# Kernel optimization log

Measured on AMD Instinct MI355X. Metric: run time of the kernel, lower is better.

Reference implementation:

```python
import jax, jax.numpy as jnp
import numpy as np

A0 = 0.529177249
SIGMA = jnp.array([0.5515909, 1.8886297, 1.3225029, 1.2316629, 2.1884933, 1.7750372, 1.3677907, 1.3820058], dtype=jnp.float32)

N_MOL, N_ATOM, AEV_LEN = 256, 384, 384
DIMS = [160, 128, 96]


def _mlp(x, W1, b1, W2, b2, W3, b3, W4, b4):
    celu = lambda v: jax.nn.celu(v, alpha=0.1)
    h = celu(x @ W1.T + b1)
    h = celu(h @ W2.T + b2)
    h = celu(h @ W3.T + b3)
    return jax.nn.softplus(h @ W4.T + b4)  # (Nn, 1)


def setup_inputs() -> dict:
    key = jax.random.key(0)
    ks = jax.random.split(key, 12)
    species = jax.random.randint(ks[0], (N_MOL, N_ATOM), 0, 8)
    # pad the tail of each molecule (species == -1)
    species = species.at[:, N_ATOM - 64:].set(-1)
    coordinates = jax.random.normal(ks[1], (N_MOL, N_ATOM, 3), dtype=jnp.float32) * 3.0
    net_charge = jax.random.normal(ks[2], (N_MOL,), dtype=jnp.float32)
    aev = jax.random.normal(ks[3], (N_MOL, N_ATOM, AEV_LEN), dtype=jnp.float32)
    in_dim = AEV_LEN + 2
    d1, d2, d3 = DIMS
    s = 0.05
    W1 = jax.random.normal(ks[4], (d1, in_dim), dtype=jnp.float32) * s
    b1 = jnp.zeros((d1,), dtype=jnp.float32)
    W2 = jax.random.normal(ks[5], (d2, d1), dtype=jnp.float32) * s
    b2 = jnp.zeros((d2,), dtype=jnp.float32)
    W3 = jax.random.normal(ks[6], (d3, d2), dtype=jnp.float32) * s
    b3 = jnp.zeros((d3,), dtype=jnp.float32)
    W4 = jax.random.normal(ks[7], (1, d3), dtype=jnp.float32) * s
    b4 = jnp.zeros((1,), dtype=jnp.float32)
    return {"species": species, "coordinates": coordinates, "net_charge": net_charge,
            "aev": aev, "W1": W1, "b1": b1, "W2": W2, "b2": b2,
            "W3": W3, "b3": b3, "W4": W4, "b4": b4}


def reference(species, coordinates, net_charge, aev, W1, b1, W2, b2, W3, b3, W4, b4):
    N, n = species.shape
    # pairwise distances in atomic units (eps avoids div-by-zero on diagonal)
    diff = coordinates[:, None, :, :] - coordinates[:, :, None, :]  # (N,n,n,3)
    distances = jnp.sqrt(jnp.sum(diff * diff, axis=-1) + 1e-16) / A0  # (N,n,n)

    padding_mask = (species != -1).astype(coordinates.dtype)  # (N,n)
    pair_mask = padding_mask[:, :, None] * padding_mask[:, None, :]  # (N,n,n)
    num_atoms = padding_mask.sum(axis=1)  # (N,)

    # ESP kernel j_ij (constant across iterations)
    sig = SIGMA[species]  # negative padding index wraps to last sigma, as in torch
    sig_sqsum = jnp.maximum(sig[:, None, :] ** 2 + sig[:, :, None] ** 2, 1e-8)
    j_ij = jax.lax.erf(distances / jnp.sqrt(2.0 * sig_sqsum)) / distances  # (N,n,n)
    diag_mask = 1.0 - jnp.eye(n, dtype=coordinates.dtype)
    j_masked = j_ij * pair_mask * diag_mask[None]  # fuse masks once

    mask_flat = species.reshape(-1) != -1  # (N*n,)
    aev_flat = aev.reshape(N * n, -1)
    pred_charges = jnp.zeros((N * n,), dtype=coordinates.dtype)
    esp = jnp.zeros((N * n,), dtype=coordinates.dtype)

    for _ in range(4):
        feats = jnp.concatenate(
            [aev_flat, pred_charges[:, None], esp[:, None]], axis=1)  # (Nn, aev+2)
        chi_all = _mlp(feats, W1, b1, W2, b2, W3, b3, W4, b4)[:, 0]
        chi = jnp.where(mask_flat, chi_all, 0.0)  # padded atoms keep 0 (masked_scatter)
        chi_copy = chi.reshape(N, n)
        chi_sum = chi_copy.sum(axis=-1)  # (N,)
        k_net = 1.0 + jnp.abs(net_charge) / chi_sum
        chi_mean = chi_sum / num_atoms
        k_p = jnp.where(net_charge > 0, k_net, 1.0)
        k_n = jnp.where(net_charge < 0, k_net, 1.0)
        iter_charges = (-k_n[:, None] * chi_copy + (k_p * chi_mean)[:, None]) * padding_mask
        # esp_j = sum_i q_i * j_ij[i, j] (masked)
        esp2d = jnp.sum(iter_charges[:, :, None] * j_masked, axis=1)  # (N,n)
        pred_charges = iter_charges.reshape(-1)
        esp = esp2d.reshape(-1)

    return species, pred_charges.reshape(N, n)
```

## Files before the change

kernel.cpp:

```cpp
#include <hip/hip_runtime.h>
#include <math.h>

#define NMOL 256
#define NATOM 384
#define NN (NMOL*NATOM)
#define A0C  0.529177249f
#define A0_INV (1.0f/0.529177249f)

typedef short bf16x8 __attribute__((ext_vector_type(8)));
typedef float f32x4  __attribute__((ext_vector_type(4)));
typedef _Float16 h16x8 __attribute__((ext_vector_type(8)));

__constant__ float c_sigma[8] = {0.5515909f, 1.8886297f, 1.3225029f, 1.2316629f,
                                 2.1884933f, 1.7750372f, 1.3677907f, 1.3820058f};

__device__ __forceinline__ short f2b(float f) {
    unsigned u = __float_as_uint(f);
    u = (u + 0x7fffu + ((u >> 16) & 1u)) >> 16;
    return (short)u;
}
__device__ __forceinline__ float b2f(short s) {
    return __uint_as_float(((unsigned)(unsigned short)s) << 16);
}
__device__ __forceinline__ float celu01(float v) {
    float e = __builtin_amdgcn_exp2f(v * 14.426950408889634f);
    return v > 0.f ? v : fmaf(0.1f, e, -0.1f);
}
__device__ __forceinline__ bf16x8 cvt8(f32x4 a, f32x4 b) {
    bf16x8 r;
    r[0] = f2b(a.x); r[1] = f2b(a.y); r[2] = f2b(a.z); r[3] = f2b(a.w);
    r[4] = f2b(b.x); r[5] = f2b(b.y); r[6] = f2b(b.z); r[7] = f2b(b.w);
    return r;
}

__device__ __forceinline__ float erf_fast(float x) {
    float t = __builtin_amdgcn_rcpf(fmaf(0.3275911f, x, 1.0f));
    float p = fmaf(t, 1.061405429f, -1.453152027f);
    p = fmaf(t, p, 1.421413741f);
    p = fmaf(t, p, -0.284496736f);
    p = fmaf(t, p, 0.254829592f);
    p = p * t;
    float e = __builtin_amdgcn_exp2f(-x * x * 1.4426950408889634f);
    return fmaf(-p, e, 1.0f);
}

template<int N, int K>
__global__ __launch_bounds__(256, 4)
void gemm0_k(const float* __restrict__ A, const short* __restrict__ Bw,
             const float* __restrict__ bias, short* __restrict__ Cout)
{
    constexpr int NK = K / 32;
    constexpr int NF = N / 32;
    constexpr int N2 = N / 2;
    constexpr int AROW = 40, BROW = 40;
    constexpr int ASZ = 64 * AROW;
    constexpr int BSZ = N * BROW;
    constexpr int AB  = 2 * ASZ + 2 * BSZ;
    constexpr int CSZ = 64 * N;
    constexpr int SM  = AB > CSZ ? AB : CSZ;
    constexpr int NB  = (N * 4 + 255) / 256;

    __shared__ short smem[SM];
    short* As0 = smem;
    short* As1 = smem + ASZ;
    short* Bs0 = smem + 2 * ASZ;
    short* Bs1 = smem + 2 * ASZ + BSZ;
    short* Cs  = smem;

    const int t    = threadIdx.x;
    const int lane = t & 63;
    const int wave = t >> 6;
    const int wm   = wave >> 1, wn = wave & 1;
    const int l15  = lane & 15, l4 = lane >> 4;
    const int m0   = blockIdx.x * 64;
    const int arow = t >> 2, aseg = t & 3;
    const float* a_f32 = A + ((size_t)m0 + arow) * K + aseg * 8;

    f32x4 af0, af1;
    bf16x8 br[NB];

    auto loadA = [&](int k0) {
        af0 = *(const f32x4*)(a_f32 + k0);
        af1 = *(const f32x4*)(a_f32 + k0 + 4);
    };
    auto loadB = [&](int k0) {
        #pragma unroll
        for (int ci = 0; ci < NB; ++ci) {
            int c = ci * 256 + t;
            if ((N * 4) % 256 == 0 || c < N * 4) {
                int row = c >> 2, half = c & 3;
                br[ci] = *(const bf16x8*)(Bw + (size_t)row * K + k0 + half * 8);
            }
        }
    };
    auto writeA = [&](short* dst) {
        *(bf16x8*)&dst[arow * AROW + aseg * 8] = cvt8(af0, af1);
    };
    auto writeB = [&](short* dst) {
        #pragma unroll
        for (int ci = 0; ci < NB; ++ci) {
            int c = ci * 256 + t;
            if ((N * 4) % 256 == 0 || c < N * 4) {
                int row = c >> 2, half = c & 3;
                *(bf16x8*)&dst[row * BROW + half * 8] = br[ci];
            }
        }
    };

    f32x4 acc[2][NF] = {};

    loadA(0); loadB(0);
    writeA(As0); writeB(Bs0);
    __syncthreads();

    int cur = 0;
    for (int ks = 0; ks < NK; ++ks) {
        if (ks + 1 < NK) { loadA((ks + 1) * 32); loadB((ks + 1) * 32); }
        short* Ac = cur ? As1 : As0;
        short* Bc = cur ? Bs1 : Bs0;
        bf16x8 a[2];
        #pragma unroll
        for (int mf = 0; mf < 2; ++mf)
            a[mf] = *(const bf16x8*)&Ac[(wm * 32 + mf * 16 + l15) * AROW + l4 * 8];
        #pragma unroll
        for (int nf = 0; nf < NF; ++nf) {
            bf16x8 b = *(const bf16x8*)&Bc[(wn * N2 + nf * 16 + l15) * BROW + l4 * 8];
            #pragma unroll
            for (int mf = 0; mf < 2; ++mf)
                acc[mf][nf] = __builtin_amdgcn_mfma_f32_16x16x32_bf16(a[mf], b, acc[mf][nf], 0, 0, 0);
        }
        if (ks + 1 < NK) {
            writeA(cur ? As0 : As1);
            writeB(cur ? Bs0 : Bs1);
            __syncthreads();
            cur ^= 1;
        }
    }
    __syncthreads();

    #pragma unroll
    for (int nf = 0; nf < NF; ++nf) {
        int col = wn * N2 + nf * 16 + l15;
        float bc = bias[col];
        #pragma unroll
        for (int mf = 0; mf < 2; ++mf)
            #pragma unroll
            for (int r = 0; r < 4; ++r)
                Cs[(wm * 32 + mf * 16 + l4 * 4 + r) * N + col] = f2b(acc[mf][nf][r] + bc);
    }
    __syncthreads();
    #pragma unroll
    for (int i = 0; i < NF; ++i) {
        int c = i * 256 + t;
        *(bf16x8*)(Cout + (size_t)m0 * N + c * 8) = *(const bf16x8*)&Cs[c * 8];
    }
}

__global__ __launch_bounds__(256, 4)
void mlp23_kernel(const short* __restrict__ h1p, const short* __restrict__ W2b,
                  const float* __restrict__ b2, const short* __restrict__ W3b,
                  const float* __restrict__ b3, const float* __restrict__ W4,
                  const float* __restrict__ b4,
                  const float* __restrict__ qv, const float* __restrict__ espv,
                  const float* __restrict__ w1qp, const float* __restrict__ w1ep,
                  const int* __restrict__ species, float* __restrict__ chi)
{
    constexpr int K1 = 160, K2 = 128, N3 = 96;
    constexpr int H2ROW = 140;

    __shared__ short H2[64 * H2ROW];
    __shared__ float wq_s[K1], we_s[K1], w4_s[N3], b3_s[N3];
    __shared__ float chp[2][64];

    const int t    = threadIdx.x;
    const int lane = t & 63;
    const int wave = t >> 6;
    const int wm   = wave >> 1, wn = wave & 1;
    const int l15  = lane & 15, l4 = lane >> 4;
    const int m0   = blockIdx.x * 64;

    if (t < K1) { wq_s[t] = w1qp[t]; we_s[t] = w1ep[t]; }
    if (t < N3) { w4_s[t] = W4[t]; b3_s[t] = b3[t]; }

    int rowg[2];
    float qrow[2], erow[2];
    #pragma unroll
    for (int mf = 0; mf < 2; ++mf) {
        rowg[mf] = m0 + wm * 32 + mf * 16 + l15;
        qrow[mf] = qv[rowg[mf]];
        erow[mf] = espv[rowg[mf]] + espv[NN + rowg[mf]]
                 + espv[2 * (size_t)NN + rowg[mf]] + espv[3 * (size_t)NN + rowg[mf]];
    }
    __syncthreads();

    f32x4 acc[2][4] = {};
    #pragma unroll
    for (int ks = 0; ks < 5; ++ks) {
        const int k0 = ks * 32 + l4 * 8;
        f32x4 wq0 = *(const f32x4*)&wq_s[k0];
        f32x4 wq1 = *(const f32x4*)&wq_s[k0 + 4];
        f32x4 we0 = *(const f32x4*)&we_s[k0];
        f32x4 we1 = *(const f32x4*)&we_s[k0 + 4];
        bf16x8 a[2];
        #pragma unroll
        for (int mf = 0; mf < 2; ++mf) {
            bf16x8 h = *(const bf16x8*)(h1p + (size_t)rowg[mf] * K1 + k0);
            #pragma unroll
            for (int j = 0; j < 4; ++j) {
                float v = b2f(h[j]) + qrow[mf] * wq0[j] + erow[mf] * we0[j];
                a[mf][j] = f2b(celu01(v));
                float v2 = b2f(h[j + 4]) + qrow[mf] * wq1[j] + erow[mf] * we1[j];
                a[mf][j + 4] = f2b(celu01(v2));
            }
        }
        #pragma unroll
        for (int nf = 0; nf < 4; ++nf) {
            bf16x8 b = *(const bf16x8*)(W2b + (size_t)(wn * 64 + nf * 16 + l15) * K1 + k0);
            #pragma unroll
            for (int mf = 0; mf < 2; ++mf)
                acc[mf][nf] = __builtin_amdgcn_mfma_f32_16x16x32_bf16(a[mf], b, acc[mf][nf], 0, 0, 0);
        }
    }

    #pragma unroll
    for (int nf = 0; nf < 4; ++nf) {
        int col = wn * 64 + nf * 16 + l15;
        float bc = b2[col];
        #pragma unroll
        for (int mf = 0; mf < 2; ++mf)
            #pragma unroll
            for (int r = 0; r < 4; ++r)
                H2[(wm * 32 + mf * 16 + l4 * 4 + r) * H2ROW + col] =
                    f2b(celu01(acc[mf][nf][r] + bc));
    }
    __syncthreads();

    f32x4 acc2[2][3] = {};
    #pragma unroll
    for (int ks = 0; ks < 4; ++ks) {
        bf16x8 a[2];
        #pragma unroll
        for (int mf = 0; mf < 2; ++mf)
            a[mf] = *(const bf16x8*)&H2[(wm * 32 + mf * 16 + l15) * H2ROW + ks * 32 + l4 * 8];
        #pragma unroll
        for (int nf = 0; nf < 3; ++nf) {
            bf16x8 b = *(const bf16x8*)(W3b + (size_t)(wn * 48 + nf * 16 + l15) * K2 + ks * 32 + l4 * 8);
            #pragma unroll
            for (int mf = 0; mf < 2; ++mf)
                acc2[mf][nf] = __builtin_amdgcn_mfma_f32_16x16x32_bf16(a[mf], b, acc2[mf][nf], 0, 0, 0);
        }
    }

    float val[2][4];
    #pragma unroll
    for (int mf = 0; mf < 2; ++mf)
        #pragma unroll
        for (int r = 0; r < 4; ++r) val[mf][r] = 0.f;
    #pragma unroll
    for (int nf = 0; nf < 3; ++nf) {
        int col = wn * 48 + nf * 16 + l15;
        float bc = b3_s[col];
        float wc = w4_s[col];
        #pragma unroll
        for (int mf = 0; mf < 2; ++mf)
            #pragma unroll
            for (int r = 0; r < 4; ++r)
                val[mf][r] += celu01(acc2[mf][nf][r] + bc) * wc;
    }
    #pragma unroll
    for (int off = 1; off < 16; off <<= 1)
        #pragma unroll
        for (int mf = 0; mf < 2; ++mf)
            #pragma unroll
            for (int r = 0; r < 4; ++r)
                val[mf][r] += __shfl_xor(val[mf][r], off, 64);
    if (l15 == 0) {
        #pragma unroll
        for (int mf = 0; mf < 2; ++mf)
            #pragma unroll
            for (int r = 0; r < 4; ++r)
                chp[wn][wm * 32 + mf * 16 + l4 * 4 + r] = val[mf][r];
    }
    __syncthreads();
    if (t < 64) {
        float s = chp[0][t] + chp[1][t] + b4[0];
        s = fmaxf(s, 0.f) + log1pf(expf(-fabsf(s)));
        chi[m0 + t] = (species[m0 + t] != -1) ? s : 0.f;
    }
}

__global__ __launch_bounds__(384)
void jbuild_kernel(const float* __restrict__ coords, const int* __restrict__ species,
                   _Float16* __restrict__ J)
{
    __shared__ float cx[NATOM], cy[NATOM], cz[NATOM], s2[NATOM], mk[NATOM];
    int m = blockIdx.x, it0 = blockIdx.y * 48;
    int j = threadIdx.x;
    int idx = m * NATOM + j;
    float rx = coords[(size_t)idx * 3 + 0];
    float ry = coords[(size_t)idx * 3 + 1];
    float rz = coords[(size_t)idx * 3 + 2];
    int sp = species[idx];
    float sig = c_sigma[sp < 0 ? 7 : sp];
    cx[j] = rx; cy[j] = ry; cz[j] = rz;
    s2[j] = sig * sig;
    float maskj = (sp != -1) ? 1.f : 0.f;
    mk[j] = maskj;
    __syncthreads();
    float s2j = s2[j];
    #pragma unroll 4
    for (int ii = 0; ii < 48; ++ii) {
        int i = it0 + ii;
        float dx = cx[i] - rx, dy = cy[i] - ry, dz = cz[i] - rz;
        float d2 = fmaf(dx, dx, fmaf(dy, dy, dz * dz)) + 1e-16f;
        float rs = __builtin_amdgcn_rsqf(d2);
        float d  = d2 * rs * A0_INV;
        float ss = fmaxf(s2[i] + s2j, 1e-8f);
        float x  = d * __builtin_amdgcn_rsqf(2.f * ss);
        float val = erf_fast(x) * rs * A0C;
        val *= maskj * mk[i];
        val = (i == j) ? 0.f : val;
        J[((size_t)m * NATOM + i) * NATOM + j] = (_Float16)val;
    }
}

template<bool DO_MV>
__global__ __launch_bounds__(384)
void espmv_kernel(const float* __restrict__ chi, const int* __restrict__ species,
                  const float* __restrict__ netq, const _Float16* __restrict__ J,
                  float* __restrict__ q, float* __restrict__ esp_part)
{
    __shared__ float pw[6], pwc[6];
    __shared__ float qs[DO_MV ? 96 : 1];
    __shared__ float part[DO_MV ? 8 : 1][DO_MV ? 384 : 1];
    int m = blockIdx.x, ic = blockIdx.y;
    int t = threadIdx.x;
    int lane = t & 63, wv = t >> 6;
    int idx = m * NATOM + t;
    float c = chi[idx];
    int sp = species[idx];
    float mask = (sp != -1) ? 1.f : 0.f;
    float sc = c, sm = mask;
    #pragma unroll
    for (int off = 1; off < 64; off <<= 1) {
        sc += __shfl_xor(sc, off, 64);
        sm += __shfl_xor(sm, off, 64);
    }
    if (lane == 0) { pw[wv] = sc; pwc[wv] = sm; }
    __syncthreads();
    float chi_sum = pw[0] + pw[1] + pw[2] + pw[3] + pw[4] + pw[5];
    float na      = pwc[0] + pwc[1] + pwc[2] + pwc[3] + pwc[4] + pwc[5];
    float Q = netq[m];
    float k_net = 1.f + fabsf(Q) / chi_sum;
    float chi_mean = chi_sum / na;
    float k_p = (Q > 0.f) ? k_net : 1.f;
    float k_n = (Q < 0.f) ? k_net : 1.f;
    float qj = (-k_n * c + k_p * chi_mean) * mask;
    if (ic == 0) q[idx] = qj;

    if (DO_MV) {
        if (t >= ic * 96 && t < ic * 96 + 96) qs[t - ic * 96] = qj;
        __syncthreads();
        int jv = t % 48, isub = t / 48;
        int j0 = jv * 8;
        float acc[8] = {};
        #pragma unroll 4
        for (int k = 0; k < 12; ++k) {
            int il = isub * 12 + k;
            int i = ic * 96 + il;
            h16x8 h = *(const h16x8*)&J[((size_t)m * NATOM + i) * NATOM + j0];
            float qi = qs[il];
            #pragma unroll
            for (int r = 0; r < 8; ++r) acc[r] = fmaf(qi, (float)h[r], acc[r]);
        }
        #pragma unroll
        for (int r = 0; r < 8; ++r) part[isub][j0 + r] = acc[r];
        __syncthreads();
        float s = 0.f;
        #pragma unroll
        for (int g = 0; g < 8; ++g) s += part[g][t];
        esp_part[(size_t)ic * NN + idx] = s;
    }
}

template<bool DO_ESP>
__global__ __launch_bounds__(384)
void espq_kernel(const float* __restrict__ chi, const int* __restrict__ species,
                 const float* __restrict__ netq, const float* __restrict__ coords,
                 float* __restrict__ q, float* __restrict__ esp)
{
    __shared__ float red[512], redc[512];
    __shared__ float cx[NATOM], cy[NATOM], cz[NATOM], s2[NATOM], qs[NATOM];
    int m = blockIdx.x, j = threadIdx.x;
    int idx = m * NATOM + j;
    float c = chi[idx];
    int sp = species[idx];
    float mask = (sp != -1) ? 1.f : 0.f;
    red[j] = c; redc[j] = mask;
    if (j < 128) { red[NATOM + j] = 0.f; redc[NATOM + j] = 0.f; }
    __syncthreads();
    for (int s = 256; s > 0; s >>= 1) {
        if (j < s) { red[j] += red[j + s]; redc[j] += redc[j + s]; }
        __syncthreads();
    }
    float chi_sum = red[0], na = redc[0];
    float Q = netq[m];
    float k_net = 1.f + fabsf(Q) / chi_sum;
    float chi_mean = chi_sum / na;
    float k_p = (Q > 0.f) ? k_net : 1.f;
    float k_n = (Q < 0.f) ? k_net : 1.f;
    float qj = (-k_n * c + k_p * chi_mean) * mask;
    q[idx] = qj;

    if (DO_ESP) {
        float rx = coords[(size_t)idx * 3 + 0];
        float ry = coords[(size_t)idx * 3 + 1];
        float rz = coords[(size_t)idx * 3 + 2];
        cx[j] = rx; cy[j] = ry; cz[j] = rz;
        float sig = c_sigma[sp < 0 ? 7 : sp];
        s2[j] = sig * sig;
        qs[j] = qj;
        __syncthreads();
        float s2j = s2[j];
        float acc = 0.f;
        for (int i = 0; i < NATOM; ++i) {
            float dx = cx[i] - rx, dy = cy[i] - ry, dz = cz[i] - rz;
            float d2 = fmaf(dx, dx, fmaf(dy, dy, dz * dz)) + 1e-16f;
            float rs = __builtin_amdgcn_rsqf(d2);
            float d  = d2 * rs * A0_INV;
            float ss = fmaxf(s2[i] + s2j, 1e-8f);
            float x  = d * __builtin_amdgcn_rsqf(2.f * ss);
            float val = erf_fast(x) * rs * A0C;
            acc += (i == j) ? 0.f : qs[i] * val;
        }
        esp[idx] = (mask != 0.f) ? acc : 0.f;
    }
}

__global__ __launch_bounds__(256)
void wcvt_kernel(const float* __restrict__ W1, const float* __restrict__ W2,
                 const float* __restrict__ W3,
                 short* __restrict__ W1b, short* __restrict__ W2b,
                 short* __restrict__ W3b, float* __restrict__ w1q,
                 float* __restrict__ w1e)
{
    int i = blockIdx.x * 256 + threadIdx.x;
    if (i < 160 * 384) {
        int r = i / 384, cc = i % 384;
        W1b[i] = f2b(W1[(size_t)r * 386 + cc]);
    }
    int j = i - 160 * 384;
    if (j >= 0 && j < 128 * 160) W2b[j] = f2b(W2[j]);
    int k2 = j - 128 * 160;
    if (k2 >= 0 && k2 < 96 * 128) W3b[k2] = f2b(W3[k2]);
    if (i < 160) {
        w1q[i] = W1[(size_t)i * 386 + 384];
        w1e[i] = W1[(size_t)i * 386 + 385];
    }
}

__global__ __launch_bounds__(256)
void out_kernel(const int* __restrict__ species, const float* __restrict__ q,
                float* __restrict__ out)
{
    int i = blockIdx.x * 256 + threadIdx.x;
    out[i] = (float)species[i];
    out[NN + i] = q[i];
}

extern "C" void kernel_launch(void* const* d_in, const int* in_sizes, int n_in,
                              void* d_out, int out_size, void* d_ws, size_t ws_size,
                              hipStream_t stream)
{
    const int*   species = (const int*)  d_in[0];
    const float* coords  = (const float*)d_in[1];
    const float* netq    = (const float*)d_in[2];
    const float* aev     = (const float*)d_in[3];
    const float* W1 = (const float*)d_in[4];
    const float* b1 = (const float*)d_in[5];
    const float* W2 = (const float*)d_in[6];
    const float* b2 = (const float*)d_in[7];
    const float* W3 = (const float*)d_in[8];
    const float* b3 = (const float*)d_in[9];
    const float* W4 = (const float*)d_in[10];
    const float* b4 = (const float*)d_in[11];

    float* q    = (float*)d_ws;
    float* chi  = q + NN;
    float* espp = chi + NN;
    float* w1q  = espp + 4 * (size_t)NN;
    float* w1e  = w1q + 160;
    short* W1b  = (short*)(w1e + 160);
    short* W2b  = W1b + 160 * 384;
    short* W3b  = W2b + 128 * 160;
    short* h1p  = W3b + 96 * 128;
    _Float16* J = (_Float16*)(h1p + (size_t)NN * 160);

    const size_t NEED = (size_t)((char*)(J + (size_t)NN * 384) - (char*)d_ws);
    const bool use_J = (ws_size >= NEED);

    hipMemsetAsync(d_ws, 0, 6 * (size_t)NN * sizeof(float), stream);
    wcvt_kernel<<<(160 * 384 + 128 * 160 + 96 * 128 + 255) / 256, 256, 0, stream>>>(
        W1, W2, W3, W1b, W2b, W3b, w1q, w1e);

    if (use_J)
        jbuild_kernel<<<dim3(NMOL, 8), 384, 0, stream>>>(coords, species, J);

    gemm0_k<160, 384><<<NN / 64, 256, 0, stream>>>(aev, W1b, b1, h1p);

    for (int it = 0; it < 4; ++it) {
        mlp23_kernel<<<NN / 64, 256, 0, stream>>>(
            h1p, W2b, b2, W3b, b3, W4, b4, q, espp, w1q, w1e, species, chi);
        if (use_J) {
            if (it < 3)
                espmv_kernel<true><<<dim3(NMOL, 4), 384, 0, stream>>>(
                    chi, species, netq, J, q, espp);
            else
                espmv_kernel<false><<<dim3(NMOL, 1), 384, 0, stream>>>(
                    chi, species, netq, J, q, espp);
        } else {
            if (it < 3)
                espq_kernel<true><<<NMOL, 384, 0, stream>>>(
                    chi, species, netq, coords, q, espp);
            else
                espq_kernel<false><<<NMOL, 384, 0, stream>>>(
                    chi, species, netq, coords, q, espp);
        }
    }

    out_kernel<<<NN / 256, 256, 0, stream>>>(species, q, (float*)d_out);
}
```

Before: 257.4 us.

## Fuse all charge-equilibration iterations into one persistent per-molecule kernel

Replaces the per-iteration launches (MLP layers 2-4, the J-matrix build, the ESP matvec, the charge update and the output write) with a single kernel that runs one block per molecule. The block keeps h1 in registers and W2/W3 in LDS, and recomputes the ESP pair kernel on the fly each iteration instead of storing a precomputed fp16 J matrix. This removes the J build, its global read traffic, the intermediate q/chi/esp global buffers and the memset, plus about a dozen launches. In exchange, only 256 blocks of 512 threads run, which may underfill the GPU, and the erf-based pair kernel is recomputed three times per molecule.

```diff
diff --git a/kernel.cpp b/kernel.cpp
--- a/kernel.cpp
+++ b/kernel.cpp
@@ -9,7 +9,6 @@
 
 typedef short bf16x8 __attribute__((ext_vector_type(8)));
 typedef float f32x4  __attribute__((ext_vector_type(4)));
-typedef _Float16 h16x8 __attribute__((ext_vector_type(8)));
 
 __constant__ float c_sigma[8] = {0.5515909f, 1.8886297f, 1.3225029f, 1.2316629f,
                                  2.1884933f, 1.7750372f, 1.3677907f, 1.3820058f};
@@ -156,284 +155,231 @@
     }
 }
 
-__global__ __launch_bounds__(256, 4)
-void mlp23_kernel(const short* __restrict__ h1p, const short* __restrict__ W2b,
-                  const float* __restrict__ b2, const short* __restrict__ W3b,
-                  const float* __restrict__ b3, const float* __restrict__ W4,
-                  const float* __restrict__ b4,
-                  const float* __restrict__ qv, const float* __restrict__ espv,
-                  const float* __restrict__ w1qp, const float* __restrict__ w1ep,
-                  const int* __restrict__ species, float* __restrict__ chi)
+#define MROW  164
+#define W3ROW 132
+
+__global__ __launch_bounds__(512, 2)
+void mega_kernel(const short* __restrict__ h1p, const short* __restrict__ W2b,
+                 const float* __restrict__ b2v, const short* __restrict__ W3b,
+                 const float* __restrict__ b3v, const float* __restrict__ W4,
+                 const float* __restrict__ b4, const float* __restrict__ w1qp,
+                 const float* __restrict__ w1ep, const int* __restrict__ species,
+                 const float* __restrict__ netq, const float* __restrict__ coords,
+                 float* __restrict__ out)
 {
-    constexpr int K1 = 160, K2 = 128, N3 = 96;
-    constexpr int H2ROW = 140;
-
-    __shared__ short H2[64 * H2ROW];
-    __shared__ float wq_s[K1], we_s[K1], w4_s[N3], b3_s[N3];
-    __shared__ float chp[2][64];
+    __shared__ short BUF[128 * MROW];
+    __shared__ short W2s[128 * MROW];
+    __shared__ short W3s[96 * W3ROW];
+    __shared__ float wq_s[160], we_s[160], b2_s[128], b3_s[96], w4_s[96];
+    __shared__ float cxs[NATOM], cys[NATOM], czs[NATOM], s2s[NATOM], msk_s[NATOM];
+    __shared__ float chi_s[NATOM], q_s[NATOM], esp_s[NATOM];
+    __shared__ float chp[2][128];
+    __shared__ float red_s[8], redc_s[8];
 
     const int t    = threadIdx.x;
     const int lane = t & 63;
-    const int wave = t >> 6;
-    const int wm   = wave >> 1, wn = wave & 1;
+    const int wv   = t >> 6;
+    const int rg   = wv >> 1;
+    const int ch   = wv & 1;
     const int l15  = lane & 15, l4 = lane >> 4;
-    const int m0   = blockIdx.x * 64;
-
-    if (t < K1) { wq_s[t] = w1qp[t]; we_s[t] = w1ep[t]; }
-    if (t < N3) { w4_s[t] = W4[t]; b3_s[t] = b3[t]; }
-
-    int rowg[2];
-    float qrow[2], erow[2];
+    const int m    = blockIdx.x;
+
+    if (t < 160)                { wq_s[t] = w1qp[t]; we_s[t] = w1ep[t]; }
+    else if (t < 288)           b2_s[t - 160] = b2v[t - 160];
+    else if (t < 384)           { b3_s[t - 288] = b3v[t - 288]; w4_s[t - 288] = W4[t - 288]; }
+    if (t < NATOM) {
+        int idx = m * NATOM + t;
+        cxs[t] = coords[(size_t)idx * 3 + 0];
+        cys[t] = coords[(size_t)idx * 3 + 1];
+        czs[t] = coords[(size_t)idx * 3 + 2];
+        int sp = species[idx];
+        float sig = c_sigma[sp < 0 ? 7 : sp];
+        s2s[t] = sig * sig;
+        msk_s[t] = (sp != -1) ? 1.f : 0.f;
+        q_s[t] = 0.f; esp_s[t] = 0.f;
+    }
     #pragma unroll
-    for (int mf = 0; mf < 2; ++mf) {
-        rowg[mf] = m0 + wm * 32 + mf * 16 + l15;
-        qrow[mf] = qv[rowg[mf]];
-        erow[mf] = espv[rowg[mf]] + espv[NN + rowg[mf]]
-                 + espv[2 * (size_t)NN + rowg[mf]] + espv[3 * (size_t)NN + rowg[mf]];
+    for (int i = 0; i < 5; ++i) {
+        int id = t + i * 512;
+        int row = id / 20, seg = id % 20;
+        *(bf16x8*)&W2s[row * MROW + seg * 8] = *(const bf16x8*)(W2b + (size_t)row * 160 + seg * 8);
+    }
+    #pragma unroll
+    for (int i = 0; i < 3; ++i) {
+        int id = t + i * 512;
+        int row = id / 16, seg = id % 16;
+        *(bf16x8*)&W3s[row * W3ROW + seg * 8] = *(const bf16x8*)(W3b + (size_t)row * 128 + seg * 8);
+    }
+
+    bf16x8 hraw[3][2][5];
+    #pragma unroll
+    for (int c = 0; c < 3; ++c) {
+        __syncthreads();
+        #pragma unroll
+        for (int i = 0; i < 5; ++i) {
+            int id = t + i * 512;
+            int row = id / 20, seg = id % 20;
+            *(bf16x8*)&BUF[row * MROW + seg * 8] =
+                *(const bf16x8*)(h1p + ((size_t)m * NATOM + c * 128 + row) * 160 + seg * 8);
+        }
+        __syncthreads();
+        #pragma unroll
+        for (int mf = 0; mf < 2; ++mf)
+            #pragma unroll
+            for (int ks = 0; ks < 5; ++ks)
+                hraw[c][mf][ks] = *(const bf16x8*)&BUF[(rg * 32 + mf * 16 + l15) * MROW + ks * 32 + l4 * 8];
     }
     __syncthreads();
 
-    f32x4 acc[2][4] = {};
-    #pragma unroll
-    for (int ks = 0; ks < 5; ++ks) {
-        const int k0 = ks * 32 + l4 * 8;
-        f32x4 wq0 = *(const f32x4*)&wq_s[k0];
-        f32x4 wq1 = *(const f32x4*)&wq_s[k0 + 4];
-        f32x4 we0 = *(const f32x4*)&we_s[k0];
-        f32x4 we1 = *(const f32x4*)&we_s[k0 + 4];
-        bf16x8 a[2];
-        #pragma unroll
-        for (int mf = 0; mf < 2; ++mf) {
-            bf16x8 h = *(const bf16x8*)(h1p + (size_t)rowg[mf] * K1 + k0);
-            #pragma unroll
-            for (int j = 0; j < 4; ++j) {
-                float v = b2f(h[j]) + qrow[mf] * wq0[j] + erow[mf] * we0[j];
-                a[mf][j] = f2b(celu01(v));
-                float v2 = b2f(h[j + 4]) + qrow[mf] * wq1[j] + erow[mf] * we1[j];
-                a[mf][j + 4] = f2b(celu01(v2));
-            }
-        }
-        #pragma unroll
-        for (int nf = 0; nf < 4; ++nf) {
-            bf16x8 b = *(const bf16x8*)(W2b + (size_t)(wn * 64 + nf * 16 + l15) * K1 + k0);
-            #pragma unroll
-            for (int mf = 0; mf < 2; ++mf)
-                acc[mf][nf] = __builtin_amdgcn_mfma_f32_16x16x32_bf16(a[mf], b, acc[mf][nf], 0, 0, 0);
-        }
-    }
-
-    #pragma unroll
-    for (int nf = 0; nf < 4; ++nf) {
-        int col = wn * 64 + nf * 16 + l15;
-        float bc = b2[col];
-        #pragma unroll
-        for (int mf = 0; mf < 2; ++mf)
-            #pragma unroll
-            for (int r = 0; r < 4; ++r)
-                H2[(wm * 32 + mf * 16 + l4 * 4 + r) * H2ROW + col] =
-                    f2b(celu01(acc[mf][nf][r] + bc));
-    }
-    __syncthreads();
-
-    f32x4 acc2[2][3] = {};
-    #pragma unroll
-    for (int ks = 0; ks < 4; ++ks) {
-        bf16x8 a[2];
-        #pragma unroll
-        for (int mf = 0; mf < 2; ++mf)
-            a[mf] = *(const bf16x8*)&H2[(wm * 32 + mf * 16 + l15) * H2ROW + ks * 32 + l4 * 8];
-        #pragma unroll
-        for (int nf = 0; nf < 3; ++nf) {
-            bf16x8 b = *(const bf16x8*)(W3b + (size_t)(wn * 48 + nf * 16 + l15) * K2 + ks * 32 + l4 * 8);
-            #pragma unroll
-            for (int mf = 0; mf < 2; ++mf)
-                acc2[mf][nf] = __builtin_amdgcn_mfma_f32_16x16x32_bf16(a[mf], b, acc2[mf][nf], 0, 0, 0);
-        }
-    }
-
-    float val[2][4];
-    #pragma unroll
-    for (int mf = 0; mf < 2; ++mf)
-        #pragma unroll
-        for (int r = 0; r < 4; ++r) val[mf][r] = 0.f;
-    #pragma unroll
-    for (int nf = 0; nf < 3; ++nf) {
-        int col = wn * 48 + nf * 16 + l15;
-        float bc = b3_s[col];
-        float wc = w4_s[col];
-        #pragma unroll
-        for (int mf = 0; mf < 2; ++mf)
-            #pragma unroll
-            for (int r = 0; r < 4; ++r)
-                val[mf][r] += celu01(acc2[mf][nf][r] + bc) * wc;
-    }
-    #pragma unroll
-    for (int off = 1; off < 16; off <<= 1)
-        #pragma unroll
-        for (int mf = 0; mf < 2; ++mf)
-            #pragma unroll
-            for (int r = 0; r < 4; ++r)
-                val[mf][r] += __shfl_xor(val[mf][r], off, 64);
-    if (l15 == 0) {
-        #pragma unroll
-        for (int mf = 0; mf < 2; ++mf)
-            #pragma unroll
-            for (int r = 0; r < 4; ++r)
-                chp[wn][wm * 32 + mf * 16 + l4 * 4 + r] = val[mf][r];
-    }
-    __syncthreads();
-    if (t < 64) {
-        float s = chp[0][t] + chp[1][t] + b4[0];
-        s = fmaxf(s, 0.f) + log1pf(expf(-fabsf(s)));
-        chi[m0 + t] = (species[m0 + t] != -1) ? s : 0.f;
-    }
-}
-
-__global__ __launch_bounds__(384)
-void jbuild_kernel(const float* __restrict__ coords, const int* __restrict__ species,
-                   _Float16* __restrict__ J)
-{
-    __shared__ float cx[NATOM], cy[NATOM], cz[NATOM], s2[NATOM], mk[NATOM];
-    int m = blockIdx.x, it0 = blockIdx.y * 48;
-    int j = threadIdx.x;
-    int idx = m * NATOM + j;
-    float rx = coords[(size_t)idx * 3 + 0];
-    float ry = coords[(size_t)idx * 3 + 1];
-    float rz = coords[(size_t)idx * 3 + 2];
-    int sp = species[idx];
-    float sig = c_sigma[sp < 0 ? 7 : sp];
-    cx[j] = rx; cy[j] = ry; cz[j] = rz;
-    s2[j] = sig * sig;
-    float maskj = (sp != -1) ? 1.f : 0.f;
-    mk[j] = maskj;
-    __syncthreads();
-    float s2j = s2[j];
-    #pragma unroll 4
-    for (int ii = 0; ii < 48; ++ii) {
-        int i = it0 + ii;
-        float dx = cx[i] - rx, dy = cy[i] - ry, dz = cz[i] - rz;
-        float d2 = fmaf(dx, dx, fmaf(dy, dy, dz * dz)) + 1e-16f;
-        float rs = __builtin_amdgcn_rsqf(d2);
-        float d  = d2 * rs * A0_INV;
-        float ss = fmaxf(s2[i] + s2j, 1e-8f);
-        float x  = d * __builtin_amdgcn_rsqf(2.f * ss);
-        float val = erf_fast(x) * rs * A0C;
-        val *= maskj * mk[i];
-        val = (i == j) ? 0.f : val;
-        J[((size_t)m * NATOM + i) * NATOM + j] = (_Float16)val;
-    }
-}
-
-template<bool DO_MV>
-__global__ __launch_bounds__(384)
-void espmv_kernel(const float* __restrict__ chi, const int* __restrict__ species,
-                  const float* __restrict__ netq, const _Float16* __restrict__ J,
-                  float* __restrict__ q, float* __restrict__ esp_part)
-{
-    __shared__ float pw[6], pwc[6];
-    __shared__ float qs[DO_MV ? 96 : 1];
-    __shared__ float part[DO_MV ? 8 : 1][DO_MV ? 384 : 1];
-    int m = blockIdx.x, ic = blockIdx.y;
-    int t = threadIdx.x;
-    int lane = t & 63, wv = t >> 6;
-    int idx = m * NATOM + t;
-    float c = chi[idx];
-    int sp = species[idx];
-    float mask = (sp != -1) ? 1.f : 0.f;
-    float sc = c, sm = mask;
-    #pragma unroll
-    for (int off = 1; off < 64; off <<= 1) {
-        sc += __shfl_xor(sc, off, 64);
-        sm += __shfl_xor(sm, off, 64);
-    }
-    if (lane == 0) { pw[wv] = sc; pwc[wv] = sm; }
-    __syncthreads();
-    float chi_sum = pw[0] + pw[1] + pw[2] + pw[3] + pw[4] + pw[5];
-    float na      = pwc[0] + pwc[1] + pwc[2] + pwc[3] + pwc[4] + pwc[5];
-    float Q = netq[m];
-    float k_net = 1.f + fabsf(Q) / chi_sum;
-    float chi_mean = chi_sum / na;
-    float k_p = (Q > 0.f) ? k_net : 1.f;
-    float k_n = (Q < 0.f) ? k_net : 1.f;
-    float qj = (-k_n * c + k_p * chi_mean) * mask;
-    if (ic == 0) q[idx] = qj;
-
-    if (DO_MV) {
-        if (t >= ic * 96 && t < ic * 96 + 96) qs[t - ic * 96] = qj;
+    const float b4v = b4[0];
+    const float Q   = netq[m];
+
+    for (int it = 0; it < 4; ++it) {
+        #pragma unroll
+        for (int c = 0; c < 3; ++c) {
+            float qrow[2], erow[2];
+            #pragma unroll
+            for (int mf = 0; mf < 2; ++mf) {
+                int rl = c * 128 + rg * 32 + mf * 16 + l15;
+                qrow[mf] = q_s[rl];
+                erow[mf] = esp_s[rl];
+            }
+            f32x4 acc[2][4] = {};
+            #pragma unroll
+            for (int ks = 0; ks < 5; ++ks) {
+                const int k0 = ks * 32 + l4 * 8;
+                f32x4 wq0 = *(const f32x4*)&wq_s[k0];
+                f32x4 wq1 = *(const f32x4*)&wq_s[k0 + 4];
+                f32x4 we0 = *(const f32x4*)&we_s[k0];
+                f32x4 we1 = *(const f32x4*)&we_s[k0 + 4];
+                bf16x8 a[2];
+                #pragma unroll
+                for (int mf = 0; mf < 2; ++mf) {
+                    bf16x8 h = hraw[c][mf][ks];
+                    #pragma unroll
+                    for (int j = 0; j < 4; ++j) {
+                        float v  = b2f(h[j])     + qrow[mf] * wq0[j] + erow[mf] * we0[j];
+                        float v2 = b2f(h[j + 4]) + qrow[mf] * wq1[j] + erow[mf] * we1[j];
+                        a[mf][j]     = f2b(celu01(v));
+                        a[mf][j + 4] = f2b(celu01(v2));
+                    }
+                }
+                #pragma unroll
+                for (int nf = 0; nf < 4; ++nf) {
+                    bf16x8 b = *(const bf16x8*)&W2s[(ch * 64 + nf * 16 + l15) * MROW + k0];
+                    #pragma unroll
+                    for (int mf = 0; mf < 2; ++mf)
+                        acc[mf][nf] = __builtin_amdgcn_mfma_f32_16x16x32_bf16(a[mf], b, acc[mf][nf], 0, 0, 0);
+                }
+            }
+            #pragma unroll
+            for (int nf = 0; nf < 4; ++nf) {
+                int col = ch * 64 + nf * 16 + l15;
+                float bc = b2_s[col];
+                #pragma unroll
+                for (int mf = 0; mf < 2; ++mf)
+                    #pragma unroll
+                    for (int r = 0; r < 4; ++r)
+                        BUF[(rg * 32 + mf * 16 + l4 * 4 + r) * MROW + col] =
+                            f2b(celu01(acc[mf][nf][r] + bc));
+            }
+            __syncthreads();
+            f32x4 acc2[2][3] = {};
+            #pragma unroll
+            for (int ks = 0; ks < 4; ++ks) {
+                bf16x8 a2[2];
+                #pragma unroll
+                for (int mf = 0; mf < 2; ++mf)
+                    a2[mf] = *(const bf16x8*)&BUF[(rg * 32 + mf * 16 + l15) * MROW + ks * 32 + l4 * 8];
+                #pragma unroll
+                for (int nf = 0; nf < 3; ++nf) {
+                    bf16x8 b = *(const bf16x8*)&W3s[(ch * 48 + nf * 16 + l15) * W3ROW + ks * 32 + l4 * 8];
+                    #pragma unroll
+                    for (int mf = 0; mf < 2; ++mf)
+                        acc2[mf][nf] = __builtin_amdgcn_mfma_f32_16x16x32_bf16(a2[mf], b, acc2[mf][nf], 0, 0, 0);
+                }
+            }
+            float val[2][4] = {};
+            #pragma unroll
+            for (int nf = 0; nf < 3; ++nf) {
+                int col = ch * 48 + nf * 16 + l15;
+                float bc = b3_s[col], wc = w4_s[col];
+                #pragma unroll
+                for (int mf = 0; mf < 2; ++mf)
+                    #pragma unroll
+                    for (int r = 0; r < 4; ++r)
+                        val[mf][r] += celu01(acc2[mf][nf][r] + bc) * wc;
+            }
+            #pragma unroll
+            for (int off = 1; off < 16; off <<= 1)
+                #pragma unroll
+                for (int mf = 0; mf < 2; ++mf)
+                    #pragma unroll
+                    for (int r = 0; r < 4; ++r)
+                        val[mf][r] += __shfl_xor(val[mf][r], off, 64);
+            if (l15 == 0) {
+                #pragma unroll
+                for (int mf = 0; mf < 2; ++mf)
+                    #pragma unroll
+                    for (int r = 0; r < 4; ++r)
+                        chp[ch][rg * 32 + mf * 16 + l4 * 4 + r] = val[mf][r];
+            }
+            __syncthreads();
+            if (t < 128) {
+                float s = chp[0][t] + chp[1][t] + b4v;
+                s = fmaxf(s, 0.f) + log1pf(expf(-fabsf(s)));
+                chi_s[c * 128 + t] = msk_s[c * 128 + t] * s;
+            }
+        }
         __syncthreads();
-        int jv = t % 48, isub = t / 48;
-        int j0 = jv * 8;
-        float acc[8] = {};
-        #pragma unroll 4
-        for (int k = 0; k < 12; ++k) {
-            int il = isub * 12 + k;
-            int i = ic * 96 + il;
-            h16x8 h = *(const h16x8*)&J[((size_t)m * NATOM + i) * NATOM + j0];
-            float qi = qs[il];
-            #pragma unroll
-            for (int r = 0; r < 8; ++r) acc[r] = fmaf(qi, (float)h[r], acc[r]);
-        }
-        #pragma unroll
-        for (int r = 0; r < 8; ++r) part[isub][j0 + r] = acc[r];
+
+        float cv = 0.f, mv = 0.f;
+        if (t < NATOM) { cv = chi_s[t]; mv = msk_s[t]; }
+        #pragma unroll
+        for (int off = 1; off < 64; off <<= 1) {
+            cv += __shfl_xor(cv, off, 64);
+            mv += __shfl_xor(mv, off, 64);
+        }
+        if (lane == 0) { red_s[wv] = cv; redc_s[wv] = mv; }
         __syncthreads();
-        float s = 0.f;
-        #pragma unroll
-        for (int g = 0; g < 8; ++g) s += part[g][t];
-        esp_part[(size_t)ic * NN + idx] = s;
-    }
-}
-
-template<bool DO_ESP>
-__global__ __launch_bounds__(384)
-void espq_kernel(const float* __restrict__ chi, const int* __restrict__ species,
-                 const float* __restrict__ netq, const float* __restrict__ coords,
-                 float* __restrict__ q, float* __restrict__ esp)
-{
-    __shared__ float red[512], redc[512];
-    __shared__ float cx[NATOM], cy[NATOM], cz[NATOM], s2[NATOM], qs[NATOM];
-    int m = blockIdx.x, j = threadIdx.x;
-    int idx = m * NATOM + j;
-    float c = chi[idx];
-    int sp = species[idx];
-    float mask = (sp != -1) ? 1.f : 0.f;
-    red[j] = c; redc[j] = mask;
-    if (j < 128) { red[NATOM + j] = 0.f; redc[NATOM + j] = 0.f; }
-    __syncthreads();
-    for (int s = 256; s > 0; s >>= 1) {
-        if (j < s) { red[j] += red[j + s]; redc[j] += redc[j + s]; }
+        float chi_sum = red_s[0] + red_s[1] + red_s[2] + red_s[3]
+                      + red_s[4] + red_s[5] + red_s[6] + red_s[7];
+        float na      = redc_s[0] + redc_s[1] + redc_s[2] + redc_s[3]
+                      + redc_s[4] + redc_s[5] + redc_s[6] + redc_s[7];
+        float k_net = 1.f + fabsf(Q) / chi_sum;
+        float chi_mean = chi_sum / na;
+        float k_p = (Q > 0.f) ? k_net : 1.f;
+        float k_n = (Q < 0.f) ? k_net : 1.f;
+        if (t < NATOM) {
+            float qj = (-k_n * chi_s[t] + k_p * chi_mean) * msk_s[t];
+            q_s[t] = qj;
+            if (it == 3) {
+                int idx = m * NATOM + t;
+                out[idx]      = (float)species[idx];
+                out[NN + idx] = qj;
+            }
+        }
         __syncthreads();
-    }
-    float chi_sum = red[0], na = redc[0];
-    float Q = netq[m];
-    float k_net = 1.f + fabsf(Q) / chi_sum;
-    float chi_mean = chi_sum / na;
-    float k_p = (Q > 0.f) ? k_net : 1.f;
-    float k_n = (Q < 0.f) ? k_net : 1.f;
-    float qj = (-k_n * c + k_p * chi_mean) * mask;
-    q[idx] = qj;
-
-    if (DO_ESP) {
-        float rx = coords[(size_t)idx * 3 + 0];
-        float ry = coords[(size_t)idx * 3 + 1];
-        float rz = coords[(size_t)idx * 3 + 2];
-        cx[j] = rx; cy[j] = ry; cz[j] = rz;
-        float sig = c_sigma[sp < 0 ? 7 : sp];
-        s2[j] = sig * sig;
-        qs[j] = qj;
-        __syncthreads();
-        float s2j = s2[j];
-        float acc = 0.f;
-        for (int i = 0; i < NATOM; ++i) {
-            float dx = cx[i] - rx, dy = cy[i] - ry, dz = cz[i] - rz;
-            float d2 = fmaf(dx, dx, fmaf(dy, dy, dz * dz)) + 1e-16f;
-            float rs = __builtin_amdgcn_rsqf(d2);
-            float d  = d2 * rs * A0_INV;
-            float ss = fmaxf(s2[i] + s2j, 1e-8f);
-            float x  = d * __builtin_amdgcn_rsqf(2.f * ss);
-            float val = erf_fast(x) * rs * A0C;
-            acc += (i == j) ? 0.f : qs[i] * val;
-        }
-        esp[idx] = (mask != 0.f) ? acc : 0.f;
+
+        if (it < 3) {
+            if (t < NATOM) {
+                float rx = cxs[t], ry = cys[t], rz = czs[t], s2j = s2s[t];
+                float acc = 0.f;
+                #pragma unroll 4
+                for (int i = 0; i < NATOM; ++i) {
+                    float dx = cxs[i] - rx, dy = cys[i] - ry, dz = czs[i] - rz;
+                    float d2 = fmaf(dx, dx, fmaf(dy, dy, dz * dz)) + 1e-16f;
+                    float rs = __builtin_amdgcn_rsqf(d2);
+                    float d  = d2 * rs * A0_INV;
+                    float ss = fmaxf(s2s[i] + s2j, 1e-8f);
+                    float x  = d * __builtin_amdgcn_rsqf(2.f * ss);
+                    float v  = erf_fast(x) * rs * A0C;
+                    acc += (i == t) ? 0.f : q_s[i] * v;
+                }
+                esp_s[t] = (msk_s[t] != 0.f) ? acc : 0.f;
+            }
+            __syncthreads();
+        }
     }
 }
 
@@ -457,15 +403,6 @@
         w1q[i] = W1[(size_t)i * 386 + 384];
         w1e[i] = W1[(size_t)i * 386 + 385];
     }
-}
-
-__global__ __launch_bounds__(256)
-void out_kernel(const int* __restrict__ species, const float* __restrict__ q,
-                float* __restrict__ out)
-{
-    int i = blockIdx.x * 256 + threadIdx.x;
-    out[i] = (float)species[i];
-    out[NN + i] = q[i];
 }
 
 extern "C" void kernel_launch(void* const* d_in, const int* in_sizes, int n_in,
@@ -485,48 +422,19 @@
     const float* W4 = (const float*)d_in[10];
     const float* b4 = (const float*)d_in[11];
 
-    float* q    = (float*)d_ws;
-    float* chi  = q + NN;
-    float* espp = chi + NN;
-    float* w1q  = espp + 4 * (size_t)NN;
+    float* w1q  = (float*)d_ws;
     float* w1e  = w1q + 160;
     short* W1b  = (short*)(w1e + 160);
     short* W2b  = W1b + 160 * 384;
     short* W3b  = W2b + 128 * 160;
     short* h1p  = W3b + 96 * 128;
-    _Float16* J = (_Float16*)(h1p + (size_t)NN * 160);
-
-    const size_t NEED = (size_t)((char*)(J + (size_t)NN * 384) - (char*)d_ws);
-    const bool use_J = (ws_size >= NEED);
-
-    hipMemsetAsync(d_ws, 0, 6 * (size_t)NN * sizeof(float), stream);
+
     wcvt_kernel<<<(160 * 384 + 128 * 160 + 96 * 128 + 255) / 256, 256, 0, stream>>>(
         W1, W2, W3, W1b, W2b, W3b, w1q, w1e);
 
-    if (use_J)
-        jbuild_kernel<<<dim3(NMOL, 8), 384, 0, stream>>>(coords, species, J);
-
     gemm0_k<160, 384><<<NN / 64, 256, 0, stream>>>(aev, W1b, b1, h1p);
 
-    for (int it = 0; it < 4; ++it) {
-        mlp23_kernel<<<NN / 64, 256, 0, stream>>>(
-            h1p, W2b, b2, W3b, b3, W4, b4, q, espp, w1q, w1e, species, chi);
-        if (use_J) {
-            if (it < 3)
-                espmv_kernel<true><<<dim3(NMOL, 4), 384, 0, stream>>>(
-                    chi, species, netq, J, q, espp);
-            else
-                espmv_kernel<false><<<dim3(NMOL, 1), 384, 0, stream>>>(
-                    chi, species, netq, J, q, espp);
-        } else {
-            if (it < 3)
-                espq_kernel<true><<<NMOL, 384, 0, stream>>>(
-                    chi, species, netq, coords, q, espp);
-            else
-                espq_kernel<false><<<NMOL, 384, 0, stream>>>(
-                    chi, species, netq, coords, q, espp);
-        }
-    }
-
-    out_kernel<<<NN / 256, 256, 0, stream>>>(species, q, (float*)d_out);
-}
+    mega_kernel<<<NMOL, 512, 0, stream>>>(
+        h1p, W2b, b2, W3b, b3, W4, b4, w1q, w1e, species, netq, coords,
+        (float*)d_out);
+}
```

Measured after the change: 405.8 us. +57.7%, slower.
